# Kernel tuning notes

Measured on AMD Instinct MI355X. Metric: run time of the kernel, lower is better.

## Reference

```python
import jax, jax.numpy as jnp
import numpy as np

N_HEADS = 16
D_MODEL = 1024
D_K = D_MODEL // N_HEADS


def setup_inputs() -> dict:
    key = jax.random.key(0)
    ks = jax.random.split(key, 7)
    B, S = 2, 2048
    init = 0.02
    return {
        "query": jax.random.normal(ks[0], (B, S, D_MODEL), dtype=jnp.float32),
        "key": jax.random.normal(ks[1], (B, S, D_MODEL), dtype=jnp.float32),
        "value": jax.random.normal(ks[2], (B, S, D_MODEL), dtype=jnp.float32),
        "W_q": jax.random.normal(ks[3], (D_MODEL, D_MODEL), dtype=jnp.float32) * init,
        "W_k": jax.random.normal(ks[4], (D_MODEL, D_MODEL), dtype=jnp.float32) * init,
        "W_v": jax.random.normal(ks[5], (D_MODEL, D_MODEL), dtype=jnp.float32) * init,
        "W_o": jax.random.normal(ks[6], (D_MODEL, D_MODEL), dtype=jnp.float32) * init,
    }


def _split_heads(x):
    # (B, S, d_model) -> (B, H, S, d_k)
    B, S, _ = x.shape
    return x.reshape(B, S, N_HEADS, D_K).transpose(0, 2, 1, 3)


def reference(query, key, value, W_q, W_k, W_v, W_o):
    scale = jnp.sqrt(jnp.asarray(D_K, dtype=query.dtype))
    # torch Linear: y = x @ W.T
    Q = _split_heads(query @ W_q.T)   # (B,H,Sq,dk)
    K = _split_heads(key @ W_k.T)     # (B,H,Sk,dk)
    V = _split_heads(value @ W_v.T)   # (B,H,Sk,dk)
    scores = jnp.einsum("bhqd,bhkd->bhqk", Q, K) / scale
    attn = jax.nn.softmax(scores, axis=-1)           # (B,H,Sq,Sk); dropout p=0 -> identity
    attn_weights = attn.mean(axis=1)                 # (B,Sq,Sk) interpretable weights
    head_out = jnp.einsum("bhqk,bhkd->bqhd", attn, V)  # (B,Sq,H,dk)
    # NOTE: the original computes a head-gating (W_h) whose result is overwritten
    # by the concat below -> dead code, omitted.
    B, Sq = head_out.shape[0], head_out.shape[1]
    out = head_out.reshape(B, Sq, D_MODEL) @ W_o.T   # (B,Sq,d_model)
    return (out, attn_weights)
```

## Files before the change

kernel.cpp:

```cpp
#include <hip/hip_runtime.h>
#include <hip/hip_bf16.h>

#define Bq 2
#define Hh 16
#define Ss 2048
#define Dm 1024
#define Dk 64
#define QSC 0.18033688f

typedef _Float16 f16x8 __attribute__((ext_vector_type(8)));
typedef _Float16 f16x4 __attribute__((ext_vector_type(4)));
typedef _Float16 f16x2 __attribute__((ext_vector_type(2)));
typedef float    f32x4 __attribute__((ext_vector_type(4)));


__device__ __forceinline__ void gl_lds16(const void* g, void* lds) {
    __builtin_amdgcn_global_load_lds(
        (const __attribute__((address_space(1))) void*)g,
        (__attribute__((address_space(3))) void*)lds, 16, 0, 0);
}

extern "C" __device__ float __ocml_exp2_f32(float);

__device__ __forceinline__ float exp2_fast(float x) {
#if __has_builtin(__builtin_amdgcn_exp2f)
    return __builtin_amdgcn_exp2f(x);
#else
    return __ocml_exp2_f32(x);
#endif
}

__device__ __forceinline__ float rcp_fast(float x) {
#if __has_builtin(__builtin_amdgcn_rcpf)
    return __builtin_amdgcn_rcpf(x);
#else
    float r; asm("v_rcp_f32 %0, %1" : "=v"(r) : "v"(x)); return r;
#endif
}

__device__ __forceinline__ f16x2 pk_f16(float a, float b) {
    return __builtin_bit_cast(f16x2, __builtin_amdgcn_cvt_pkrtz(a, b));
}

__global__ __launch_bounds__(256) void convert_kernel(
    const float* __restrict__ q, const float* __restrict__ k,
    const float* __restrict__ v, const float* __restrict__ wq,
    const float* __restrict__ wk, const float* __restrict__ wv,
    const float* __restrict__ wo,
    _Float16* __restrict__ qd, _Float16* __restrict__ kd,
    _Float16* __restrict__ vd, _Float16* __restrict__ wd)
{
    int seg = blockIdx.y;
    const float* src; _Float16* dst; int n4;
    switch (seg) {
        case 0: src = q; dst = qd; n4 = 1048576; break;
        case 1: src = k; dst = kd; n4 = 1048576; break;
        case 2: src = v; dst = vd; n4 = 1048576; break;
        default:
            src = (seg == 3) ? wq : (seg == 4) ? wk : (seg == 5) ? wv : wo;
            dst = wd + (size_t)(seg - 3) * 1048576;
            n4 = 262144;
    }
    for (int i = blockIdx.x * 256 + threadIdx.x; i < n4; i += gridDim.x * 256) {
        float4 x = ((const float4*)src)[i];
        f16x4 h = {(_Float16)x.x, (_Float16)x.y, (_Float16)x.z, (_Float16)x.w};
        ((f16x4*)dst)[i] = h;
    }
}

__global__ __launch_bounds__(256) void gemm_qkv(
    const _Float16* __restrict__ qf, const _Float16* __restrict__ kf,
    const _Float16* __restrict__ vf, const _Float16* __restrict__ Wh,
    _Float16* __restrict__ Qd, _Float16* __restrict__ Kd,
    _Float16* __restrict__ Vd)
{
    __shared__ alignas(16) char smem[32768];
    _Float16* As = (_Float16*)smem;
    _Float16* Ws = (_Float16*)(smem + 8192);
    int z = blockIdx.z;
    const _Float16* A = (z == 0) ? qf : (z == 1) ? kf : vf;
    const _Float16* W = Wh + (size_t)z * (Dm * Dm);
    int t = threadIdx.x, lane = t & 63, w = t >> 6;
    int quad = lane >> 4, l15 = lane & 15;
    int wm = w & 1, wn = w >> 1;
    int n0 = blockIdx.x * 128, m0 = blockIdx.y * 128;

    f32x4 acc[4][4] = {};
    for (int k0 = 0; k0 < Dm; k0 += 32) {
        __syncthreads();
        for (int j = 0; j < 2; ++j) {
            int ca = w * 128 + j * 64 + lane;
            int row = ca >> 2, c8 = (ca & 3) * 8;
            gl_lds16(&A[(size_t)(m0 + row) * Dm + k0 + c8],
                     &As[(size_t)(w * 128 + j * 64) * 8]);
            gl_lds16(&W[(size_t)(n0 + row) * Dm + k0 + c8],
                     &Ws[(size_t)(w * 128 + j * 64) * 8]);
        }
        __syncthreads();
        f16x8 af[4], bf[4];
        for (int mi = 0; mi < 4; ++mi)
            af[mi] = *(const f16x8*)&As[(wm * 64 + mi * 16 + l15) * 32 + quad * 8];
        for (int ni = 0; ni < 4; ++ni)
            bf[ni] = *(const f16x8*)&Ws[(wn * 64 + ni * 16 + l15) * 32 + quad * 8];
        for (int mi = 0; mi < 4; ++mi)
            for (int ni = 0; ni < 4; ++ni)
                acc[mi][ni] = __builtin_amdgcn_mfma_f32_16x16x32_f16(
                    af[mi], bf[ni], acc[mi][ni], 0, 0, 0);
    }

    if (z == 2) {
        __syncthreads();
        for (int mi = 0; mi < 4; ++mi)
            for (int ni = 0; ni < 4; ++ni) {
                int n_l = wn * 64 + ni * 16 + l15;
                int m_b = wm * 64 + mi * 16 + quad * 4;
                f16x4 hv = {(_Float16)acc[mi][ni][0], (_Float16)acc[mi][ni][1],
                            (_Float16)acc[mi][ni][2], (_Float16)acc[mi][ni][3]};
                *(f16x4*)(smem + n_l * 256 + ((m_b * 2) ^ ((n_l & 7) << 4))) = hv;
            }
        __syncthreads();
        int b = m0 >> 11, sb = m0 & (Ss - 1);
        for (int p = 0; p < 8; ++p) {
            int cid = p * 256 + t;
            int rown = cid >> 4, c16 = cid & 15;
            f16x8 v = *(const f16x8*)(smem + rown * 256 +
                                      ((c16 * 16) ^ ((rown & 7) << 4)));
            int n = n0 + rown;
            int h = n >> 6, d = n & 63;
            *(f16x8*)&Vd[(((size_t)(b * Hh + h) * Dk + d) << 11) + sb + c16 * 8] = v;
        }
    } else {
        _Float16* Y = (z == 0) ? Qd : Kd;
        float osc = (z == 0) ? QSC : 1.0f;
        for (int mi = 0; mi < 4; ++mi)
            for (int ni = 0; ni < 4; ++ni)
                for (int r = 0; r < 4; ++r) {
                    int m = m0 + wm * 64 + mi * 16 + quad * 4 + r;
                    int n = n0 + wn * 64 + ni * 16 + l15;
                    int b = m >> 11, s = m & (Ss - 1);
                    int h = n >> 6,  d = n & 63;
                    Y[(((size_t)(b * Hh + h) * Ss + s) << 6) + d] =
                        (_Float16)(acc[mi][ni][r] * osc);
                }
    }
}

__global__ __launch_bounds__(256) void gemm_out(
    const _Float16* __restrict__ HO, const _Float16* __restrict__ Woh,
    float* __restrict__ out)
{
    __shared__ _Float16 As[128 * 32];
    __shared__ _Float16 Ws[64 * 32];
    int t = threadIdx.x, lane = t & 63, w = t >> 6;
    int quad = lane >> 4, l15 = lane & 15;
    int n0 = blockIdx.x * 64, m0 = blockIdx.y * 128;

    f32x4 acc[2][4] = {};
    for (int k0 = 0; k0 < Dm; k0 += 32) {
        __syncthreads();
        for (int j = 0; j < 2; ++j) {
            int ca = w * 128 + j * 64 + lane;
            int row = ca >> 2, c8 = (ca & 3) * 8;
            gl_lds16(&HO[(size_t)(m0 + row) * Dm + k0 + c8],
                     &As[(size_t)(w * 128 + j * 64) * 8]);
        }
        {
            int cw = w * 64 + lane;
            int row = cw >> 2, c8 = (cw & 3) * 8;
            gl_lds16(&Woh[(size_t)(n0 + row) * Dm + k0 + c8],
                     &Ws[(size_t)(w * 64) * 8]);
        }
        __syncthreads();
        f16x8 af[2], bf[4];
        for (int mi = 0; mi < 2; ++mi)
            af[mi] = *(const f16x8*)&As[(w * 32 + mi * 16 + l15) * 32 + quad * 8];
        for (int ni = 0; ni < 4; ++ni)
            bf[ni] = *(const f16x8*)&Ws[(ni * 16 + l15) * 32 + quad * 8];
        for (int mi = 0; mi < 2; ++mi)
            for (int ni = 0; ni < 4; ++ni)
                acc[mi][ni] = __builtin_amdgcn_mfma_f32_16x16x32_f16(
                    af[mi], bf[ni], acc[mi][ni], 0, 0, 0);
    }
    for (int mi = 0; mi < 2; ++mi)
        for (int ni = 0; ni < 4; ++ni)
            for (int r = 0; r < 4; ++r) {
                int m = m0 + w * 32 + mi * 16 + quad * 4 + r;
                int n = n0 + ni * 16 + l15;
                out[(size_t)m * Dm + n] = acc[mi][ni][r];
            }
}

__global__ __launch_bounds__(256) void flash_kernel(
    const _Float16* __restrict__ Qh, const _Float16* __restrict__ Kh,
    const _Float16* __restrict__ Vt, _Float16* __restrict__ Op,
    float* __restrict__ lp)
{
    __shared__ alignas(16) char Ks[8192];
    __shared__ alignas(16) char Vs[8192];
    __shared__ alignas(16) char Ps[4][4096];
    int t = threadIdx.x;
    int lane = t & 63, w = t >> 6;
    int quad = lane >> 4, l15 = lane & 15;
    int bh = blockIdx.x;
    int q0 = blockIdx.y * 128 + w * 32;
    int ks = blockIdx.z;
    int kt0 = ks * 16, kt1 = kt0 + 16;

    const _Float16* Qp = Qh + (size_t)bh * Ss * Dk;
    const _Float16* Kp = Kh + (size_t)bh * Ss * Dk;
    const _Float16* Vp = Vt + (size_t)bh * Dk * Ss;

    f16x8 qf[2][2];
#pragma unroll
    for (int qh = 0; qh < 2; ++qh)
#pragma unroll
        for (int kf = 0; kf < 2; ++kf)
            qf[qh][kf] = *(const f16x8*)
                &Qp[(size_t)(q0 + qh * 16 + l15) * Dk + kf * 32 + quad * 8];

    const _Float16 one = (_Float16)1.0f;
    const f16x8 ones = {one, one, one, one, one, one, one, one};

    int srow0 = t >> 3;
    int colh  = (t & 7) * 8;
    int sw0 = srow0 * 128 + ((colh * 2) ^ ((srow0 & 7) << 4));
    int sw1 = sw0 + 32 * 128;
    int swz = (l15 & 7) << 4;

    f16x8 kr0 = *(const f16x8*)&Kp[(size_t)(kt0 * 64 + srow0) * Dk + colh];
    f16x8 kr1 = *(const f16x8*)&Kp[(size_t)(kt0 * 64 + srow0 + 32) * Dk + colh];
    f16x8 vr0 = *(const f16x8*)&Vp[(size_t)srow0 * Ss + kt0 * 64 + colh];
    f16x8 vr1 = *(const f16x8*)&Vp[(size_t)(srow0 + 32) * Ss + kt0 * 64 + colh];

    f32x4 o_acc[2][4] = {};
    f32x4 l_acc[2] = {};
    char* Pw = Ps[w];

    for (int kt = kt0; kt < kt1; ++kt) {
        __syncthreads();
        *(f16x8*)(Ks + sw0) = kr0;
        *(f16x8*)(Ks + sw1) = kr1;
        *(f16x8*)(Vs + sw0) = vr0;
        *(f16x8*)(Vs + sw1) = vr1;
        if (kt + 1 < kt1) {
            kr0 = *(const f16x8*)&Kp[(size_t)((kt + 1) * 64 + srow0) * Dk + colh];
            kr1 = *(const f16x8*)&Kp[(size_t)((kt + 1) * 64 + srow0 + 32) * Dk + colh];
            vr0 = *(const f16x8*)&Vp[(size_t)srow0 * Ss + (kt + 1) * 64 + colh];
            vr1 = *(const f16x8*)&Vp[(size_t)(srow0 + 32) * Ss + (kt + 1) * 64 + colh];
        }
        __syncthreads();

#pragma unroll
        for (int nt = 0; nt < 4; ++nt) {
            const char* rb = Ks + ((nt * 16 + l15) << 7);
            f16x8 kf0 = *(const f16x8*)(rb + ((quad * 16) ^ swz));
            f16x8 kf1 = *(const f16x8*)(rb + ((64 + quad * 16) ^ swz));
#pragma unroll
            for (int qh = 0; qh < 2; ++qh) {
                f32x4 z = {};
                z = __builtin_amdgcn_mfma_f32_16x16x32_f16(kf0, qf[qh][0], z, 0, 0, 0);
                z = __builtin_amdgcn_mfma_f32_16x16x32_f16(kf1, qf[qh][1], z, 0, 0, 0);
                f16x2 h0 = pk_f16(exp2_fast(z[0]), exp2_fast(z[1]));
                f16x2 h1 = pk_f16(exp2_fast(z[2]), exp2_fast(z[3]));
                f16x4 hv = {h0[0], h0[1], h1[0], h1[1]};
                int prow = qh * 16 + l15;
                *(f16x4*)(Pw + prow * 128 +
                          (((nt * 32 + quad * 8)) ^ ((prow & 7) << 4))) = hv;
            }
        }

        f16x8 vf[4][2];
#pragma unroll
        for (int dt = 0; dt < 4; ++dt) {
            const char* rb = Vs + ((dt * 16 + l15) << 7);
            vf[dt][0] = *(const f16x8*)(rb + ((quad * 16) ^ swz));
            vf[dt][1] = *(const f16x8*)(rb + ((64 + quad * 16) ^ swz));
        }
#pragma unroll
        for (int qh = 0; qh < 2; ++qh) {
            const char* pr = Pw + ((qh * 16 + l15) << 7);
            f16x8 pf0 = *(const f16x8*)(pr + ((quad * 16) ^ swz));
            f16x8 pf1 = *(const f16x8*)(pr + ((64 + quad * 16) ^ swz));
            l_acc[qh] = __builtin_amdgcn_mfma_f32_16x16x32_f16(
                pf0, ones, l_acc[qh], 0, 0, 0);
            l_acc[qh] = __builtin_amdgcn_mfma_f32_16x16x32_f16(
                pf1, ones, l_acc[qh], 0, 0, 0);
#pragma unroll
            for (int dt = 0; dt < 4; ++dt) {
                o_acc[qh][dt] = __builtin_amdgcn_mfma_f32_16x16x32_f16(
                    pf0, vf[dt][0], o_acc[qh][dt], 0, 0, 0);
                o_acc[qh][dt] = __builtin_amdgcn_mfma_f32_16x16x32_f16(
                    pf1, vf[dt][1], o_acc[qh][dt], 0, 0, 0);
            }
        }
    }

    _Float16* Od = Op + (size_t)ks * (Bq * Hh * Ss * Dk) + (size_t)bh * Ss * Dk;
#pragma unroll
    for (int qh = 0; qh < 2; ++qh) {
#pragma unroll
        for (int dt = 0; dt < 4; ++dt)
#pragma unroll
            for (int r = 0; r < 4; ++r) {
                int q = q0 + qh * 16 + quad * 4 + r;
                Od[(size_t)q * Dk + dt * 16 + l15] = (_Float16)o_acc[qh][dt][r];
            }
        if (l15 == 0)
#pragma unroll
            for (int r = 0; r < 4; ++r)
                lp[(size_t)ks * 65536 + (size_t)bh * Ss + q0 + qh * 16 +
                   quad * 4 + r] = l_acc[qh][r];
    }
}

__global__ __launch_bounds__(256) void reduce_kernel(
    const _Float16* __restrict__ Op, const float* __restrict__ lp,
    _Float16* __restrict__ HO, float* __restrict__ lw)
{
    int i = blockIdx.x * 256 + threadIdx.x;
    int d4  = i & 15;
    int row = i >> 4;
    f16x4 a = ((const f16x4*)Op)[i];
    f16x4 b = ((const f16x4*)Op)[i + 1048576];
    float l = lp[row] + lp[65536 + row];
    float inv = rcp_fast(l);
    int bh = row >> 11, q = row & (Ss - 1);
    int b_ = bh >> 4,  h = bh & 15;
    f16x4 o;
    for (int j = 0; j < 4; ++j)
        o[j] = (_Float16)(((float)a[j] + (float)b[j]) * inv);
    *(f16x4*)&HO[((size_t)(b_ * Ss + q)) * Dm + h * Dk + d4 * 4] = o;
    if (d4 == 0) lw[row] = l;
}

__global__ __launch_bounds__(256) void attn_mean_kernel(
    const _Float16* __restrict__ Qh, const _Float16* __restrict__ Kh,
    const float* __restrict__ lw, float* __restrict__ out_attn)
{
    __shared__ alignas(16) char Ks[8192];
    int t = threadIdx.x;
    int lane = t & 63, w = t >> 6;
    int quad = lane >> 4, l15 = lane & 15;
    int k0 = blockIdx.x * 64;
    int q0 = blockIdx.y * 128;
    int b  = blockIdx.z;
    int qrow = q0 + w * 32;

    int srow0 = t >> 3;
    int colh  = (t & 7) * 8;
    int sw0 = srow0 * 128 + ((colh * 2) ^ ((srow0 & 7) << 4));
    int sw1 = sw0 + 32 * 128;
    int swz = (l15 & 7) << 4;

    f16x8 kr0, kr1, qn[2][2];
    float4 ln[2];
    {
        size_t base = (size_t)(b * Hh) * Ss;
        kr0 = *(const f16x8*)&Kh[(base + k0 + srow0) * Dk + colh];
        kr1 = *(const f16x8*)&Kh[(base + k0 + srow0 + 32) * Dk + colh];
#pragma unroll
        for (int qh = 0; qh < 2; ++qh) {
            qn[qh][0] = *(const f16x8*)&Qh[(base + qrow + qh * 16 + l15) * Dk + quad * 8];
            qn[qh][1] = *(const f16x8*)&Qh[(base + qrow + qh * 16 + l15) * Dk + 32 + quad * 8];
            ln[qh] = *(const float4*)&lw[base + qrow + qh * 16 + quad * 4];
        }
    }

    f32x4 acc[2][4] = {};
    for (int h = 0; h < Hh; ++h) {
        __syncthreads();
        *(f16x8*)(Ks + sw0) = kr0;
        *(f16x8*)(Ks + sw1) = kr1;
        f16x8 qf[2][2];
        float4 lv[2];
#pragma unroll
        for (int qh = 0; qh < 2; ++qh) {
            qf[qh][0] = qn[qh][0]; qf[qh][1] = qn[qh][1]; lv[qh] = ln[qh];
        }
        if (h < Hh - 1) {
            size_t base = (size_t)(b * Hh + h + 1) * Ss;
            kr0 = *(const f16x8*)&Kh[(base + k0 + srow0) * Dk + colh];
            kr1 = *(const f16x8*)&Kh[(base + k0 + srow0 + 32) * Dk + colh];
#pragma unroll
            for (int qh = 0; qh < 2; ++qh) {
                qn[qh][0] = *(const f16x8*)&Qh[(base + qrow + qh * 16 + l15) * Dk + quad * 8];
                qn[qh][1] = *(const f16x8*)&Qh[(base + qrow + qh * 16 + l15) * Dk + 32 + quad * 8];
                ln[qh] = *(const float4*)&lw[base + qrow + qh * 16 + quad * 4];
            }
        }
        __syncthreads();

        float ir[2][4];
#pragma unroll
        for (int qh = 0; qh < 2; ++qh) {
            ir[qh][0] = rcp_fast(lv[qh].x); ir[qh][1] = rcp_fast(lv[qh].y);
            ir[qh][2] = rcp_fast(lv[qh].z); ir[qh][3] = rcp_fast(lv[qh].w);
        }
#pragma unroll
        for (int nt = 0; nt < 4; ++nt) {
            const char* rb = Ks + ((nt * 16 + l15) << 7);
            f16x8 b0 = *(const f16x8*)(rb + ((quad * 16) ^ swz));
            f16x8 b1 = *(const f16x8*)(rb + ((64 + quad * 16) ^ swz));
#pragma unroll
            for (int qh = 0; qh < 2; ++qh) {
                f32x4 z = {};
                z = __builtin_amdgcn_mfma_f32_16x16x32_f16(qf[qh][0], b0, z, 0, 0, 0);
                z = __builtin_amdgcn_mfma_f32_16x16x32_f16(qf[qh][1], b1, z, 0, 0, 0);
#pragma unroll
                for (int r = 0; r < 4; ++r)
                    acc[qh][nt][r] += exp2_fast(z[r]) * ir[qh][r];
            }
        }
    }

#pragma unroll
    for (int qh = 0; qh < 2; ++qh)
#pragma unroll
        for (int nt = 0; nt < 4; ++nt)
#pragma unroll
            for (int r = 0; r < 4; ++r) {
                int q = qrow + qh * 16 + quad * 4 + r;
                out_attn[((size_t)(b * Ss + q)) * Ss + k0 + nt * 16 + l15] =
                    acc[qh][nt][r] * (1.0f / Hh);
            }
}

extern "C" void kernel_launch(void* const* d_in, const int* in_sizes, int n_in,
                              void* d_out, int out_size, void* d_ws, size_t ws_size,
                              hipStream_t stream) {
    const float* query = (const float*)d_in[0];
    const float* key   = (const float*)d_in[1];
    const float* value = (const float*)d_in[2];
    const float* Wq    = (const float*)d_in[3];
    const float* Wk    = (const float*)d_in[4];
    const float* Wv    = (const float*)d_in[5];
    const float* Wo    = (const float*)d_in[6];

    float* out      = (float*)d_out;
    float* attn_out = out + (size_t)4194304;

    _Float16* HO  = (_Float16*)attn_out;
    _Float16* qf  = (_Float16*)(attn_out + 2097152);
    _Float16* kf  = qf + 4194304;
    _Float16* vf  = kf + 4194304;
    _Float16* Op  = qf;
    float*    lp  = (float*)(Op + 2 * 4194304);

    _Float16* Qh = (_Float16*)d_ws;
    _Float16* Kh = Qh + (size_t)4194304;
    _Float16* Vt = Kh + (size_t)4194304;
    _Float16* Wh = Vt + (size_t)4194304;
    float*    lw = (float*)(Wh + (size_t)4194304);

    convert_kernel<<<dim3(256, 7), 256, 0, stream>>>(
        query, key, value, Wq, Wk, Wv, Wo, qf, kf, vf, Wh);

    gemm_qkv<<<dim3(8, 32, 3), 256, 0, stream>>>(qf, kf, vf, Wh, Qh, Kh, Vt);

    flash_kernel<<<dim3(Bq * Hh, Ss / 128, 2), 256, 0, stream>>>(Qh, Kh, Vt, Op, lp);

    reduce_kernel<<<4096, 256, 0, stream>>>(Op, lp, HO, lw);

    gemm_out<<<dim3(16, 32), 256, 0, stream>>>(HO, Wh + (size_t)3 * 1048576, out);

    attn_mean_kernel<<<dim3(Ss / 64, Ss / 128, Bq), 256, 0, stream>>>(
        Qh, Kh, lw, attn_out);
}
```

Before: 269.9 us.

## Load K and V MFMA fragments directly from global memory, dropping LDS staging

In the flash and attention-mean kernels, K and V tiles are no longer staged through shared memory with register prefetch and block barriers. Each wave now loads its MFMA fragments straight from global memory, relying on L1/L2 to serve the data the four waves share. This removes the two __syncthreads per iteration and the LDS traffic, but each wave reissues the same global loads and loses the software prefetch, which can expose memory latency.

Result: slower. 391.2 us (+45.0%).

```diff
diff --git a/kernel.cpp b/kernel.cpp
--- a/kernel.cpp
+++ b/kernel.cpp
@@ -195,8 +195,6 @@
     const _Float16* __restrict__ Vt, _Float16* __restrict__ Op,
     float* __restrict__ lp)
 {
-    __shared__ alignas(16) char Ks[8192];
-    __shared__ alignas(16) char Vs[8192];
     __shared__ alignas(16) char Ps[4][4096];
     int t = threadIdx.x;
     int lane = t & 63, w = t >> 6;
@@ -221,40 +219,26 @@
     const _Float16 one = (_Float16)1.0f;
     const f16x8 ones = {one, one, one, one, one, one, one, one};
 
-    int srow0 = t >> 3;
-    int colh  = (t & 7) * 8;
-    int sw0 = srow0 * 128 + ((colh * 2) ^ ((srow0 & 7) << 4));
-    int sw1 = sw0 + 32 * 128;
     int swz = (l15 & 7) << 4;
-
-    f16x8 kr0 = *(const f16x8*)&Kp[(size_t)(kt0 * 64 + srow0) * Dk + colh];
-    f16x8 kr1 = *(const f16x8*)&Kp[(size_t)(kt0 * 64 + srow0 + 32) * Dk + colh];
-    f16x8 vr0 = *(const f16x8*)&Vp[(size_t)srow0 * Ss + kt0 * 64 + colh];
-    f16x8 vr1 = *(const f16x8*)&Vp[(size_t)(srow0 + 32) * Ss + kt0 * 64 + colh];
 
     f32x4 o_acc[2][4] = {};
     f32x4 l_acc[2] = {};
     char* Pw = Ps[w];
 
     for (int kt = kt0; kt < kt1; ++kt) {
-        __syncthreads();
-        *(f16x8*)(Ks + sw0) = kr0;
-        *(f16x8*)(Ks + sw1) = kr1;
-        *(f16x8*)(Vs + sw0) = vr0;
-        *(f16x8*)(Vs + sw1) = vr1;
-        if (kt + 1 < kt1) {
-            kr0 = *(const f16x8*)&Kp[(size_t)((kt + 1) * 64 + srow0) * Dk + colh];
-            kr1 = *(const f16x8*)&Kp[(size_t)((kt + 1) * 64 + srow0 + 32) * Dk + colh];
-            vr0 = *(const f16x8*)&Vp[(size_t)srow0 * Ss + (kt + 1) * 64 + colh];
-            vr1 = *(const f16x8*)&Vp[(size_t)(srow0 + 32) * Ss + (kt + 1) * 64 + colh];
-        }
-        __syncthreads();
+        f16x8 vf[4][2];
+#pragma unroll
+        for (int dt = 0; dt < 4; ++dt) {
+            const _Float16* vr = &Vp[(size_t)(dt * 16 + l15) * Ss + kt * 64];
+            vf[dt][0] = *(const f16x8*)(vr + quad * 8);
+            vf[dt][1] = *(const f16x8*)(vr + 32 + quad * 8);
+        }
 
 #pragma unroll
         for (int nt = 0; nt < 4; ++nt) {
-            const char* rb = Ks + ((nt * 16 + l15) << 7);
-            f16x8 kf0 = *(const f16x8*)(rb + ((quad * 16) ^ swz));
-            f16x8 kf1 = *(const f16x8*)(rb + ((64 + quad * 16) ^ swz));
+            const _Float16* kr = &Kp[(size_t)(kt * 64 + nt * 16 + l15) * Dk];
+            f16x8 kf0 = *(const f16x8*)(kr + quad * 8);
+            f16x8 kf1 = *(const f16x8*)(kr + 32 + quad * 8);
 #pragma unroll
             for (int qh = 0; qh < 2; ++qh) {
                 f32x4 z = {};
@@ -269,13 +253,6 @@
             }
         }
 
-        f16x8 vf[4][2];
-#pragma unroll
-        for (int dt = 0; dt < 4; ++dt) {
-            const char* rb = Vs + ((dt * 16 + l15) << 7);
-            vf[dt][0] = *(const f16x8*)(rb + ((quad * 16) ^ swz));
-            vf[dt][1] = *(const f16x8*)(rb + ((64 + quad * 16) ^ swz));
-        }
 #pragma unroll
         for (int qh = 0; qh < 2; ++qh) {
             const char* pr = Pw + ((qh * 16 + l15) << 7);
@@ -337,7 +314,6 @@
     const _Float16* __restrict__ Qh, const _Float16* __restrict__ Kh,
     const float* __restrict__ lw, float* __restrict__ out_attn)
 {
-    __shared__ alignas(16) char Ks[8192];
     int t = threadIdx.x;
     int lane = t & 63, w = t >> 6;
     int quad = lane >> 4, l15 = lane & 15;
@@ -346,61 +322,25 @@
     int b  = blockIdx.z;
     int qrow = q0 + w * 32;
 
-    int srow0 = t >> 3;
-    int colh  = (t & 7) * 8;
-    int sw0 = srow0 * 128 + ((colh * 2) ^ ((srow0 & 7) << 4));
-    int sw1 = sw0 + 32 * 128;
-    int swz = (l15 & 7) << 4;
-
-    f16x8 kr0, kr1, qn[2][2];
-    float4 ln[2];
-    {
-        size_t base = (size_t)(b * Hh) * Ss;
-        kr0 = *(const f16x8*)&Kh[(base + k0 + srow0) * Dk + colh];
-        kr1 = *(const f16x8*)&Kh[(base + k0 + srow0 + 32) * Dk + colh];
-#pragma unroll
-        for (int qh = 0; qh < 2; ++qh) {
-            qn[qh][0] = *(const f16x8*)&Qh[(base + qrow + qh * 16 + l15) * Dk + quad * 8];
-            qn[qh][1] = *(const f16x8*)&Qh[(base + qrow + qh * 16 + l15) * Dk + 32 + quad * 8];
-            ln[qh] = *(const float4*)&lw[base + qrow + qh * 16 + quad * 4];
-        }
-    }
-
     f32x4 acc[2][4] = {};
     for (int h = 0; h < Hh; ++h) {
-        __syncthreads();
-        *(f16x8*)(Ks + sw0) = kr0;
-        *(f16x8*)(Ks + sw1) = kr1;
+        size_t base = (size_t)(b * Hh + h) * Ss;
         f16x8 qf[2][2];
-        float4 lv[2];
+        float ir[2][4];
 #pragma unroll
         for (int qh = 0; qh < 2; ++qh) {
-            qf[qh][0] = qn[qh][0]; qf[qh][1] = qn[qh][1]; lv[qh] = ln[qh];
-        }
-        if (h < Hh - 1) {
-            size_t base = (size_t)(b * Hh + h + 1) * Ss;
-            kr0 = *(const f16x8*)&Kh[(base + k0 + srow0) * Dk + colh];
-            kr1 = *(const f16x8*)&Kh[(base + k0 + srow0 + 32) * Dk + colh];
-#pragma unroll
-            for (int qh = 0; qh < 2; ++qh) {
-                qn[qh][0] = *(const f16x8*)&Qh[(base + qrow + qh * 16 + l15) * Dk + quad * 8];
-                qn[qh][1] = *(const f16x8*)&Qh[(base + qrow + qh * 16 + l15) * Dk + 32 + quad * 8];
-                ln[qh] = *(const float4*)&lw[base + qrow + qh * 16 + quad * 4];
-            }
-        }
-        __syncthreads();
-
-        float ir[2][4];
-#pragma unroll
-        for (int qh = 0; qh < 2; ++qh) {
-            ir[qh][0] = rcp_fast(lv[qh].x); ir[qh][1] = rcp_fast(lv[qh].y);
-            ir[qh][2] = rcp_fast(lv[qh].z); ir[qh][3] = rcp_fast(lv[qh].w);
+            const _Float16* qr = &Qh[(base + qrow + qh * 16 + l15) * Dk];
+            qf[qh][0] = *(const f16x8*)(qr + quad * 8);
+            qf[qh][1] = *(const f16x8*)(qr + 32 + quad * 8);
+            float4 lv = *(const float4*)&lw[base + qrow + qh * 16 + quad * 4];
+            ir[qh][0] = rcp_fast(lv.x); ir[qh][1] = rcp_fast(lv.y);
+            ir[qh][2] = rcp_fast(lv.z); ir[qh][3] = rcp_fast(lv.w);
         }
 #pragma unroll
         for (int nt = 0; nt < 4; ++nt) {
-            const char* rb = Ks + ((nt * 16 + l15) << 7);
-            f16x8 b0 = *(const f16x8*)(rb + ((quad * 16) ^ swz));
-            f16x8 b1 = *(const f16x8*)(rb + ((64 + quad * 16) ^ swz));
+            const _Float16* kr = &Kh[(base + k0 + nt * 16 + l15) * Dk];
+            f16x8 b0 = *(const f16x8*)(kr + quad * 8);
+            f16x8 b1 = *(const f16x8*)(kr + 32 + quad * 8);
 #pragma unroll
             for (int qh = 0; qh < 2; ++qh) {
                 f32x4 z = {};
```

## Keep attention probabilities in registers using 32x32 MFMA and permlane swaps

Applied to the files above, without the earlier changes.

Rewrites the flash attention inner loop to use 32x32x16 MFMA tiles, computing S^T so the exp'd probabilities can be repacked into the B-operand layout for the PV MFMA via v_permlane32_swap. This removes the per-tile LDS round trip for P and the ones-vector MFMA used for row sums, which are now accumulated with scalar adds plus one cross-half shuffle. The output is staged through LDS to allow 16-byte coalesced stores. It relies on the gfx950 permlane32_swap instruction and a precise lane layout, and it raises accumulator register usage.

Result: slower. 282.1 us (+4.5%).

```diff
diff --git a/kernel.cpp b/kernel.cpp
--- a/kernel.cpp
+++ b/kernel.cpp
@@ -12,6 +12,8 @@
 typedef _Float16 f16x4 __attribute__((ext_vector_type(4)));
 typedef _Float16 f16x2 __attribute__((ext_vector_type(2)));
 typedef float    f32x4 __attribute__((ext_vector_type(4)));
+typedef float    f32x16 __attribute__((ext_vector_type(16)));
+typedef unsigned int u32x4 __attribute__((ext_vector_type(4)));
 
 
 __device__ __forceinline__ void gl_lds16(const void* g, void* lds) {
@@ -38,8 +40,12 @@
 #endif
 }
 
-__device__ __forceinline__ f16x2 pk_f16(float a, float b) {
-    return __builtin_bit_cast(f16x2, __builtin_amdgcn_cvt_pkrtz(a, b));
+__device__ __forceinline__ unsigned int pk_u32(float a, float b) {
+    return __builtin_bit_cast(unsigned int, __builtin_amdgcn_cvt_pkrtz(a, b));
+}
+
+__device__ __forceinline__ void plane32_swap(unsigned int& a, unsigned int& b) {
+    asm volatile("v_permlane32_swap_b32 %0, %1" : "+v"(a), "+v"(b));
 }
 
 __global__ __launch_bounds__(256) void convert_kernel(
@@ -197,10 +203,10 @@
 {
     __shared__ alignas(16) char Ks[8192];
     __shared__ alignas(16) char Vs[8192];
-    __shared__ alignas(16) char Ps[4][4096];
+    __shared__ alignas(16) char Ot[4][4096];
     int t = threadIdx.x;
     int lane = t & 63, w = t >> 6;
-    int quad = lane >> 4, l15 = lane & 15;
+    int hi = lane >> 5, l31 = lane & 31;
     int bh = blockIdx.x;
     int q0 = blockIdx.y * 128 + w * 32;
     int ks = blockIdx.z;
@@ -210,31 +216,24 @@
     const _Float16* Kp = Kh + (size_t)bh * Ss * Dk;
     const _Float16* Vp = Vt + (size_t)bh * Dk * Ss;
 
-    f16x8 qf[2][2];
-#pragma unroll
-    for (int qh = 0; qh < 2; ++qh)
-#pragma unroll
-        for (int kf = 0; kf < 2; ++kf)
-            qf[qh][kf] = *(const f16x8*)
-                &Qp[(size_t)(q0 + qh * 16 + l15) * Dk + kf * 32 + quad * 8];
-
-    const _Float16 one = (_Float16)1.0f;
-    const f16x8 ones = {one, one, one, one, one, one, one, one};
+    f16x8 qB[4];
+#pragma unroll
+    for (int dblk = 0; dblk < 4; ++dblk)
+        qB[dblk] = *(const f16x8*)&Qp[(size_t)(q0 + l31) * Dk + dblk * 16 + hi * 8];
 
     int srow0 = t >> 3;
     int colh  = (t & 7) * 8;
     int sw0 = srow0 * 128 + ((colh * 2) ^ ((srow0 & 7) << 4));
     int sw1 = sw0 + 32 * 128;
-    int swz = (l15 & 7) << 4;
+    int swzr = (l31 & 7) << 4;
 
     f16x8 kr0 = *(const f16x8*)&Kp[(size_t)(kt0 * 64 + srow0) * Dk + colh];
     f16x8 kr1 = *(const f16x8*)&Kp[(size_t)(kt0 * 64 + srow0 + 32) * Dk + colh];
     f16x8 vr0 = *(const f16x8*)&Vp[(size_t)srow0 * Ss + kt0 * 64 + colh];
     f16x8 vr1 = *(const f16x8*)&Vp[(size_t)(srow0 + 32) * Ss + kt0 * 64 + colh];
 
-    f32x4 o_acc[2][4] = {};
-    f32x4 l_acc[2] = {};
-    char* Pw = Ps[w];
+    f32x16 oacc[2] = {};
+    float lsum = 0.f;
 
     for (int kt = kt0; kt < kt1; ++kt) {
         __syncthreads();
@@ -250,67 +249,68 @@
         }
         __syncthreads();
 
-#pragma unroll
-        for (int nt = 0; nt < 4; ++nt) {
-            const char* rb = Ks + ((nt * 16 + l15) << 7);
-            f16x8 kf0 = *(const f16x8*)(rb + ((quad * 16) ^ swz));
-            f16x8 kf1 = *(const f16x8*)(rb + ((64 + quad * 16) ^ swz));
-#pragma unroll
-            for (int qh = 0; qh < 2; ++qh) {
-                f32x4 z = {};
-                z = __builtin_amdgcn_mfma_f32_16x16x32_f16(kf0, qf[qh][0], z, 0, 0, 0);
-                z = __builtin_amdgcn_mfma_f32_16x16x32_f16(kf1, qf[qh][1], z, 0, 0, 0);
-                f16x2 h0 = pk_f16(exp2_fast(z[0]), exp2_fast(z[1]));
-                f16x2 h1 = pk_f16(exp2_fast(z[2]), exp2_fast(z[3]));
-                f16x4 hv = {h0[0], h0[1], h1[0], h1[1]};
-                int prow = qh * 16 + l15;
-                *(f16x4*)(Pw + prow * 128 +
-                          (((nt * 32 + quad * 8)) ^ ((prow & 7) << 4))) = hv;
-            }
-        }
-
-        f16x8 vf[4][2];
-#pragma unroll
-        for (int dt = 0; dt < 4; ++dt) {
-            const char* rb = Vs + ((dt * 16 + l15) << 7);
-            vf[dt][0] = *(const f16x8*)(rb + ((quad * 16) ^ swz));
-            vf[dt][1] = *(const f16x8*)(rb + ((64 + quad * 16) ^ swz));
-        }
-#pragma unroll
-        for (int qh = 0; qh < 2; ++qh) {
-            const char* pr = Pw + ((qh * 16 + l15) << 7);
-            f16x8 pf0 = *(const f16x8*)(pr + ((quad * 16) ^ swz));
-            f16x8 pf1 = *(const f16x8*)(pr + ((64 + quad * 16) ^ swz));
-            l_acc[qh] = __builtin_amdgcn_mfma_f32_16x16x32_f16(
-                pf0, ones, l_acc[qh], 0, 0, 0);
-            l_acc[qh] = __builtin_amdgcn_mfma_f32_16x16x32_f16(
-                pf1, ones, l_acc[qh], 0, 0, 0);
-#pragma unroll
-            for (int dt = 0; dt < 4; ++dt) {
-                o_acc[qh][dt] = __builtin_amdgcn_mfma_f32_16x16x32_f16(
-                    pf0, vf[dt][0], o_acc[qh][dt], 0, 0, 0);
-                o_acc[qh][dt] = __builtin_amdgcn_mfma_f32_16x16x32_f16(
-                    pf1, vf[dt][1], o_acc[qh][dt], 0, 0, 0);
-            }
-        }
-    }
-
+        unsigned int bf[4][4];
+#pragma unroll
+        for (int kb = 0; kb < 2; ++kb) {
+            f32x16 C = {};
+            const char* rb = Ks + ((kb * 32 + l31) << 7);
+#pragma unroll
+            for (int dblk = 0; dblk < 4; ++dblk) {
+                f16x8 kf = *(const f16x8*)(rb + ((dblk * 32 + hi * 16) ^ swzr));
+                C = __builtin_amdgcn_mfma_f32_32x32x16_f16(kf, qB[dblk], C, 0, 0, 0);
+            }
+#pragma unroll
+            for (int h = 0; h < 2; ++h) {
+                float p0 = exp2_fast(C[h * 8 + 0]), p1 = exp2_fast(C[h * 8 + 1]);
+                float p2 = exp2_fast(C[h * 8 + 2]), p3 = exp2_fast(C[h * 8 + 3]);
+                float p4 = exp2_fast(C[h * 8 + 4]), p5 = exp2_fast(C[h * 8 + 5]);
+                float p6 = exp2_fast(C[h * 8 + 6]), p7 = exp2_fast(C[h * 8 + 7]);
+                lsum += ((p0 + p1) + (p2 + p3)) + ((p4 + p5) + (p6 + p7));
+                unsigned int d01 = pk_u32(p0, p1), d23 = pk_u32(p2, p3);
+                unsigned int d45 = pk_u32(p4, p5), d67 = pk_u32(p6, p7);
+                plane32_swap(d01, d45);
+                plane32_swap(d23, d67);
+                int kblk = kb * 2 + h;
+                bf[kblk][0] = d01; bf[kblk][1] = d23;
+                bf[kblk][2] = d45; bf[kblk][3] = d67;
+            }
+        }
+
+#pragma unroll
+        for (int kblk = 0; kblk < 4; ++kblk) {
+            u32x4 pb = {bf[kblk][0], bf[kblk][1], bf[kblk][2], bf[kblk][3]};
+            f16x8 pB = __builtin_bit_cast(f16x8, pb);
+#pragma unroll
+            for (int d2 = 0; d2 < 2; ++d2) {
+                const char* rb = Vs + ((d2 * 32 + l31) << 7);
+                f16x8 vA = *(const f16x8*)(rb + ((kblk * 32 + hi * 16) ^ swzr));
+                oacc[d2] = __builtin_amdgcn_mfma_f32_32x32x16_f16(
+                    vA, pB, oacc[d2], 0, 0, 0);
+            }
+        }
+    }
+
+    lsum += __shfl_xor(lsum, 32);
+
+    char* Ow = Ot[w];
+#pragma unroll
+    for (int d2 = 0; d2 < 2; ++d2)
+#pragma unroll
+        for (int g = 0; g < 4; ++g) {
+            f16x4 hv = {(_Float16)oacc[d2][g * 4 + 0], (_Float16)oacc[d2][g * 4 + 1],
+                        (_Float16)oacc[d2][g * 4 + 2], (_Float16)oacc[d2][g * 4 + 3]};
+            int d = d2 * 32 + g * 8 + hi * 4;
+            *(f16x4*)(Ow + l31 * 128 + ((d * 2) ^ swzr)) = hv;
+        }
+    __syncthreads();
     _Float16* Od = Op + (size_t)ks * (Bq * Hh * Ss * Dk) + (size_t)bh * Ss * Dk;
 #pragma unroll
-    for (int qh = 0; qh < 2; ++qh) {
-#pragma unroll
-        for (int dt = 0; dt < 4; ++dt)
-#pragma unroll
-            for (int r = 0; r < 4; ++r) {
-                int q = q0 + qh * 16 + quad * 4 + r;
-                Od[(size_t)q * Dk + dt * 16 + l15] = (_Float16)o_acc[qh][dt][r];
-            }
-        if (l15 == 0)
-#pragma unroll
-            for (int r = 0; r < 4; ++r)
-                lp[(size_t)ks * 65536 + (size_t)bh * Ss + q0 + qh * 16 +
-                   quad * 4 + r] = l_acc[qh][r];
-    }
+    for (int i = 0; i < 4; ++i) {
+        f16x8 v = *(const f16x8*)(Ow + l31 * 128 + ((hi * 64 + i * 16) ^ swzr));
+        *(f16x8*)&Od[(size_t)(q0 + l31) * Dk + hi * 32 + i * 8] = v;
+    }
+    if (lane < 32)
+        lp[(size_t)ks * 65536 + (size_t)bh * Ss + q0 + l31] = lsum;
 }
 
 __global__ __launch_bounds__(256) void reduce_kernel(
```
